# Performance work log

Hardware: AMD Instinct MI355X
Metric: run time of the kernel (lower is better)

## Reference

```python
import jax, jax.numpy as jnp
import numpy as np

NEG_SLOPE = 0.2  # PyG GATConv default leaky_relu slope
N_NODES, N_EDGES, F_IN, HID = 25000, 200000, 64, 128


def gat_layer(x, src, dst, W, a_src, a_dst, b, heads, ch):
    """PyG-style GATConv (concat=True, eval mode). x:[N,Fin] -> [N,heads*ch]."""
    N = x.shape[0]
    h = (x @ W).reshape(N, heads, ch)                      # [N,H,C]
    al_s = jnp.sum(h * a_src, axis=-1)                     # [N,H]
    al_d = jnp.sum(h * a_dst, axis=-1)                     # [N,H]
    e = jax.nn.leaky_relu(al_s[src] + al_d[dst], NEG_SLOPE)  # [E,H]
    # segment softmax over incoming edges of each dst node (stable)
    e = e - jax.ops.segment_max(e, dst, num_segments=N)[dst]
    ex = jnp.exp(e)
    alpha = ex / jax.ops.segment_sum(ex, dst, num_segments=N)[dst]  # [E,H]
    out = jax.ops.segment_sum(h[src] * alpha[:, :, None], dst, num_segments=N)  # [N,H,C]
    return out.reshape(N, heads * ch) + b


def setup_inputs() -> dict:
    key = jax.random.key(0)
    ks = jax.random.split(key, 24)
    def g(k, shape, fan_in):
        return jax.random.normal(k, shape, dtype=jnp.float32) / np.sqrt(fan_in)
    inp = {
        "x": jax.random.normal(ks[0], (N_NODES, F_IN), dtype=jnp.float32),
        "edge_index": jax.random.randint(ks[1], (2, N_EDGES), 0, N_NODES, dtype=jnp.int64) if jax.config.jax_enable_x64 else jax.random.randint(ks[1], (2, N_EDGES), 0, N_NODES).astype(jnp.int32),
        "liquor_idx": jax.random.randint(ks[2], (4096,), 0, N_NODES),
        "ingredient_idx": jax.random.randint(ks[3], (4096,), 0, N_NODES),
        "W1": g(ks[4], (F_IN, 8 * HID), F_IN), "a_s1": g(ks[5], (8, HID), HID), "a_d1": g(ks[6], (8, HID), HID), "b1": jnp.zeros((8 * HID,), jnp.float32),
        "W2": g(ks[7], (8 * HID, 8 * HID), 8 * HID), "a_s2": g(ks[8], (8, HID), HID), "a_d2": g(ks[9], (8, HID), HID), "b2": jnp.zeros((8 * HID,), jnp.float32),
        "W3": g(ks[10], (8 * HID, HID), 8 * HID), "a_s3": g(ks[11], (1, HID), HID), "a_d3": g(ks[12], (1, HID), HID), "b3": jnp.zeros((HID,), jnp.float32),
        # MLP scorer: 256 -> 128 -> 64 -> 1
        "mw1": g(ks[13], (2 * HID, HID), 2 * HID), "mb1": jnp.zeros((HID,), jnp.float32),
        "mw2": g(ks[14], (HID, HID // 2), HID), "mb2": jnp.zeros((HID // 2,), jnp.float32),
        "mw3": g(ks[15], (HID // 2, 1), HID // 2), "mb3": jnp.zeros((1,), jnp.float32),
    }
    return inp


def reference(x, edge_index, liquor_idx, ingredient_idx,
              W1, a_s1, a_d1, b1, W2, a_s2, a_d2, b2, W3, a_s3, a_d3, b3,
              mw1, mb1, mw2, mb2, mw3, mb3):
    N = x.shape[0]
    loops = jnp.arange(N, dtype=edge_index.dtype)  # GATConv adds self-loops
    src = jnp.concatenate([edge_index[0], loops])
    dst = jnp.concatenate([edge_index[1], loops])
    h = jax.nn.relu(gat_layer(x, src, dst, W1, a_s1, a_d1, b1, 8, HID))
    h = jax.nn.relu(gat_layer(h, src, dst, W2, a_s2, a_d2, b2, 8, HID))
    h = gat_layer(h, src, dst, W3, a_s3, a_d3, b3, 1, HID)
    pair = jnp.concatenate([h[liquor_idx], h[ingredient_idx]], axis=-1)  # [B,256]
    z = jax.nn.relu(pair @ mw1 + mb1)
    z = jax.nn.relu(z @ mw2 + mb2)
    z = z @ mw3 + mb3
    return jax.nn.sigmoid(z).squeeze(-1)
```

## Files before the change

kernel.cpp:

```cpp
#include <hip/hip_runtime.h>
#include <math.h>

#define NEG_SLOPE 0.2f

typedef short short8 __attribute__((ext_vector_type(8)));
typedef float f32x4 __attribute__((ext_vector_type(4)));

__device__ __forceinline__ float lrelu(float x){ return x > 0.f ? x : NEG_SLOPE * x; }

__device__ __forceinline__ unsigned short f2bf(float f){
  union { float f; unsigned u; } v; v.f = f;
  unsigned r = v.u + 0x7fff + ((v.u >> 16) & 1);
  return (unsigned short)(r >> 16);
}
__device__ __forceinline__ float bf2f(unsigned short u){
  union { unsigned u; float f; } v; v.u = ((unsigned)u) << 16; return v.f;
}

__device__ __forceinline__ void gld16(const unsigned short* g, unsigned short* l){
  __builtin_amdgcn_global_load_lds(
      (const __attribute__((address_space(1))) unsigned int*)g,
      (__attribute__((address_space(3))) unsigned int*)l, 16, 0, 0);
}

#define MFMA_BF16 __builtin_amdgcn_mfma_f32_16x16x32_bf16

__global__ void k_count(const int* __restrict__ dst, int* __restrict__ cnt, int E){
  int e = blockIdx.x*blockDim.x + threadIdx.x;
  if (e < E) atomicAdd(&cnt[dst[e]], 1);
}

__global__ void k_blockscan(const int* __restrict__ cnt, int* __restrict__ row,
                            int* __restrict__ aux, int n){
  __shared__ int buf[256];
  int t = threadIdx.x;
  int base = blockIdx.x * 256;
  int v = (base + t < n) ? cnt[base + t] : 0;
  buf[t] = v;
  __syncthreads();
  #pragma unroll
  for (int off = 1; off < 256; off <<= 1){
    int u = (t >= off) ? buf[t - off] : 0;
    __syncthreads();
    buf[t] += u;
    __syncthreads();
  }
  if (base + t < n) row[base + t + 1] = buf[t];
  if (t == 255) aux[blockIdx.x] = buf[255];
  if (blockIdx.x == 0 && t == 0) row[0] = 0;
}

__global__ void k_addoff(const int* __restrict__ aux, int* __restrict__ row, int n){
  __shared__ int s_pre;
  int b = blockIdx.x, t = threadIdx.x;
  if (t == 0){
    int pre = 0;
    for (int i = 0; i < b; ++i) pre += aux[i];
    s_pre = pre;
  }
  __syncthreads();
  int i = b * 256 + t;
  if (i < n) row[i + 1] += s_pre;
}

__global__ void k_scatter(const int* __restrict__ src, const int* __restrict__ dst,
                          const int* __restrict__ row, int* __restrict__ cur,
                          int* __restrict__ csr, int E){
  int e = blockIdx.x*blockDim.x + threadIdx.x;
  if (e < E){
    int d = dst[e];
    int p = atomicAdd(&cur[d], 1);
    csr[row[d] + p] = src[e];
  }
}

__global__ void k_prep(const float* __restrict__ x, unsigned short* __restrict__ xb, int nx, int nxb,
                       const float* __restrict__ W1, unsigned short* __restrict__ Wt1,
                       const float* __restrict__ W2, unsigned short* __restrict__ Wt2,
                       const float* __restrict__ W3, unsigned short* __restrict__ Wt3){
  __shared__ float tile[32][33];
  int b = blockIdx.x, t = threadIdx.x;
  if (b < nxb){
    int i0 = b * 2048 + t * 8;
    if (i0 + 8 <= nx){
      float4 f0 = *reinterpret_cast<const float4*>(x + i0);
      float4 f1 = *reinterpret_cast<const float4*>(x + i0 + 4);
      short8 o;
      o[0]=f2bf(f0.x); o[1]=f2bf(f0.y); o[2]=f2bf(f0.z); o[3]=f2bf(f0.w);
      o[4]=f2bf(f1.x); o[5]=f2bf(f1.y); o[6]=f2bf(f1.z); o[7]=f2bf(f1.w);
      *reinterpret_cast<short8*>(xb + i0) = o;
    } else {
      for (int k = 0; k < 8 && i0 + k < nx; ++k) xb[i0 + k] = f2bf(x[i0 + k]);
    }
    return;
  }
  const float* W; unsigned short* Wt; int K, N, ti;
  if (b < nxb + 64)            { W = W1; Wt = Wt1; K = 64;   N = 1024; ti = b - nxb;
                                 int kb = (ti & 1) * 32, nb = (ti >> 1) * 32;
                                 int tx = t & 31, ty = t >> 5;
                                 #pragma unroll
                                 for (int i = ty; i < 32; i += 8) tile[i][tx] = W[(size_t)(kb+i)*N + nb+tx];
                                 __syncthreads();
                                 #pragma unroll
                                 for (int i = ty; i < 32; i += 8) Wt[(size_t)(nb+i)*K + kb+tx] = f2bf(tile[tx][i]);
                                 return; }
  if (b < nxb + 64 + 1024)     { W = W2; Wt = Wt2; K = 1024; N = 1024; ti = b - nxb - 64; }
  else                         { W = W3; Wt = Wt3; K = 1024; N = 128;  ti = b - nxb - 64 - 1024; }
  int kb = (ti & 31) * 32, nb = (ti >> 5) * 32;
  int tx = t & 31, ty = t >> 5;
  #pragma unroll
  for (int i = ty; i < 32; i += 8) tile[i][tx] = W[(size_t)(kb+i)*N + nb+tx];
  __syncthreads();
  #pragma unroll
  for (int i = ty; i < 32; i += 8) Wt[(size_t)(nb+i)*K + kb+tx] = f2bf(tile[tx][i]);
}

__global__ void k_fold(const float* __restrict__ W1, const float* __restrict__ a_s,
                       const float* __restrict__ a_d, float* __restrict__ ws){
  int k = blockIdx.x, t = threadIdx.x;
  int h = t >> 5, l = t & 31;
  float4 wv = *reinterpret_cast<const float4*>(&W1[(size_t)k * 1024 + h * 128 + l * 4]);
  float4 sv = *reinterpret_cast<const float4*>(&a_s[h * 128 + l * 4]);
  float4 dv = *reinterpret_cast<const float4*>(&a_d[h * 128 + l * 4]);
  float ps = wv.x*sv.x + wv.y*sv.y + wv.z*sv.z + wv.w*sv.w;
  float pd = wv.x*dv.x + wv.y*dv.y + wv.z*dv.z + wv.w*dv.w;
  #pragma unroll
  for (int off = 16; off >= 1; off >>= 1){
    ps += __shfl_xor(ps, off);
    pd += __shfl_xor(pd, off);
  }
  if (l == 0){ ws[k * 16 + h] = ps; ws[k * 16 + 8 + h] = pd; }
}

__global__ void k_logits1(const unsigned short* __restrict__ xb, const float* __restrict__ ws,
                          float* __restrict__ ALS, float* __restrict__ ALD, int N){
  __shared__ unsigned short lx[32 * 64];
  __shared__ float lw[64 * 16];
  int t = threadIdx.x;
  int n0 = blockIdx.x * 32;
  int r = t >> 3, c = (t & 7) * 8;
  if (n0 + r < N)
    *reinterpret_cast<short8*>(&lx[r * 64 + c]) =
      *reinterpret_cast<const short8*>(&xb[(size_t)(n0 + r) * 64 + c]);
  else {
    short8 z = {0,0,0,0,0,0,0,0};
    *reinterpret_cast<short8*>(&lx[r * 64 + c]) = z;
  }
  *reinterpret_cast<float4*>(&lw[t * 4]) = *reinterpret_cast<const float4*>(&ws[t * 4]);
  __syncthreads();
  int nl = t >> 3, h = t & 7;
  if (n0 + nl >= N) return;
  float s = 0.f, d = 0.f;
  #pragma unroll 8
  for (int k = 0; k < 64; ++k){
    float xv = bf2f(lx[nl * 64 + k]);
    s = fmaf(xv, lw[k * 16 + h], s);
    d = fmaf(xv, lw[k * 16 + 8 + h], d);
  }
  ALS[(size_t)(n0 + nl) * 8 + h] = s;
  ALD[(size_t)(n0 + nl) * 8 + h] = d;
}

__global__ void k_gat_x(const unsigned short* __restrict__ xb, const float* __restrict__ ALS,
                        const float* __restrict__ ALD, const int* __restrict__ row,
                        const int* __restrict__ csr, unsigned short* __restrict__ G, int N){
  int t = threadIdx.x;
  int n = blockIdx.x * 4 + (t >> 6);
  if (n >= N) return;
  int lane = t & 63;
  float ald[8], m[8], l[8], acc[8];
  float xv = bf2f(xb[(size_t)n * 64 + lane]);
  #pragma unroll
  for (int h = 0; h < 8; ++h){
    ald[h] = ALD[(size_t)n * 8 + h];
    m[h] = lrelu(ALS[(size_t)n * 8 + h] + ald[h]);
    l[h] = 1.f;
    acc[h] = xv;
  }
  int beg = row[n], end = row[n + 1];
  for (int j = beg; j < end; ++j){
    int s = csr[j];
    float xs = bf2f(xb[(size_t)s * 64 + lane]);
    #pragma unroll
    for (int h = 0; h < 8; ++h){
      float e = lrelu(ALS[(size_t)s * 8 + h] + ald[h]);
      float mn = fmaxf(m[h], e);
      float sc = __expf(m[h] - mn);
      float p  = __expf(e - mn);
      acc[h] = acc[h] * sc + p * xs;
      l[h]   = l[h] * sc + p;
      m[h]   = mn;
    }
  }
  #pragma unroll
  for (int h = 0; h < 8; ++h)
    G[(size_t)n * 512 + h * 64 + lane] = f2bf(acc[h] / l[h]);
}

__global__ __launch_bounds__(256) void k_gemm_g(
    const unsigned short* __restrict__ G,
    const unsigned short* __restrict__ Bt,
    const float* __restrict__ bias,
    unsigned short* __restrict__ C,
    int M){
  __shared__ unsigned short As[128 * 32];
  __shared__ unsigned short Bs[128 * 32];
  const int nwg = gridDim.x;
  int bid = blockIdx.x;
  int swz = ((nwg & 7) == 0) ? ((bid & 7) * (nwg >> 3) + (bid >> 3)) : bid;
  const int head = swz % 8, byi = swz / 8;
  const int bm = byi * 128, bn = head * 128;
  const int tid  = threadIdx.x;
  const int lane = tid & 63, wave = tid >> 6;
  const int wr = wave >> 1, wc = wave & 1;
  const int lr = lane & 15, lk = lane >> 4;
  const int srow = wave * 16 + (lane >> 2);
  const int skc  = (lane & 3) * 8;
  int ar0 = bm + srow;      if (ar0 >= M) ar0 = M - 1;
  int ar1 = bm + srow + 64; if (ar1 >= M) ar1 = M - 1;
  const unsigned short* ga0 = G + (size_t)ar0 * 512 + head * 64 + skc;
  const unsigned short* ga1 = G + (size_t)ar1 * 512 + head * 64 + skc;
  const unsigned short* gb0 = Bt + (size_t)(bn + srow) * 64 + skc;
  const unsigned short* gb1 = Bt + (size_t)(bn + srow + 64) * 64 + skc;
  f32x4 acc[4][4] = {};
  #pragma unroll
  for (int k0 = 0; k0 < 64; k0 += 32){
    gld16(ga0 + k0, &As[(size_t)wave * 512]);
    gld16(ga1 + k0, &As[(size_t)(wave + 4) * 512]);
    gld16(gb0 + k0, &Bs[(size_t)wave * 512]);
    gld16(gb1 + k0, &Bs[(size_t)(wave + 4) * 512]);
    __syncthreads();
    short8 af[4], bg[4];
    #pragma unroll
    for (int m = 0; m < 4; ++m)
      af[m] = *reinterpret_cast<const short8*>(&As[(wr * 64 + m * 16 + lr) * 32 + lk * 8]);
    #pragma unroll
    for (int n = 0; n < 4; ++n)
      bg[n] = *reinterpret_cast<const short8*>(&Bs[(wc * 64 + n * 16 + lr) * 32 + lk * 8]);
    #pragma unroll
    for (int m = 0; m < 4; ++m)
      #pragma unroll
      for (int n = 0; n < 4; ++n)
        acc[m][n] = MFMA_BF16(af[m], bg[n], acc[m][n], 0, 0, 0);
    __syncthreads();
  }
  float bv[4];
  #pragma unroll
  for (int n = 0; n < 4; ++n) bv[n] = bias[bn + wc * 64 + n * 16 + lr];
  #pragma unroll
  for (int m = 0; m < 4; ++m){
    #pragma unroll
    for (int j = 0; j < 4; ++j){
      int rowi = bm + wr * 64 + m * 16 + lk * 4 + j;
      if (rowi < M){
        #pragma unroll
        for (int n = 0; n < 4; ++n)
          C[(size_t)rowi * 1024 + bn + wc * 64 + n * 16 + lr] = f2bf(fmaxf(acc[m][n][j] + bv[n], 0.f));
      }
    }
  }
}

template<int HEADS>
__global__ __launch_bounds__(256) void k_gemm_fused(
    const unsigned short* __restrict__ A, const unsigned short* __restrict__ Bt,
    unsigned short* __restrict__ C,
    const float* __restrict__ a_s, const float* __restrict__ a_d,
    float* __restrict__ ALS, float* __restrict__ ALD,
    int M, int N, int K, int gxc){
  __shared__ unsigned short SMEM[2 * 128 * 32];
  unsigned short* As = SMEM;
  unsigned short* Bs = SMEM + 128 * 32;
  const int nwg = gridDim.x;
  int bid = blockIdx.x;
  int swz = ((nwg & 7) == 0) ? ((bid & 7) * (nwg >> 3) + (bid >> 3)) : bid;
  const int bxi = swz % gxc, byi = swz / gxc;
  const int bm = byi * 128, bn = bxi * 128;
  const int head = bxi;
  const int tid  = threadIdx.x;
  const int lane = tid & 63, wave = tid >> 6;
  const int wr = wave >> 1, wc = wave & 1;
  const int lr = lane & 15, lk = lane >> 4;
  const int srow = wave * 16 + (lane >> 2);
  const int skc  = (lane & 3) * 8;
  int ar0 = bm + srow;      if (ar0 >= M) ar0 = M - 1;
  int ar1 = bm + srow + 64; if (ar1 >= M) ar1 = M - 1;
  const unsigned short* ga0 = A  + (size_t)ar0 * K + skc;
  const unsigned short* ga1 = A  + (size_t)ar1 * K + skc;
  const unsigned short* gb0 = Bt + (size_t)(bn + srow) * K + skc;
  const unsigned short* gb1 = Bt + (size_t)(bn + srow + 64) * K + skc;
  f32x4 acc[4][4] = {};
  for (int k0 = 0; k0 < K; k0 += 32){
    gld16(ga0 + k0, &As[(size_t)wave * 512]);
    gld16(ga1 + k0, &As[(size_t)(wave + 4) * 512]);
    gld16(gb0 + k0, &Bs[(size_t)wave * 512]);
    gld16(gb1 + k0, &Bs[(size_t)(wave + 4) * 512]);
    __syncthreads();
    short8 af[4], bg[4];
    #pragma unroll
    for (int m = 0; m < 4; ++m)
      af[m] = *reinterpret_cast<const short8*>(&As[(wr * 64 + m * 16 + lr) * 32 + lk * 8]);
    #pragma unroll
    for (int n = 0; n < 4; ++n)
      bg[n] = *reinterpret_cast<const short8*>(&Bs[(wc * 64 + n * 16 + lr) * 32 + lk * 8]);
    #pragma unroll
    for (int m = 0; m < 4; ++m)
      #pragma unroll
      for (int n = 0; n < 4; ++n)
        acc[m][n] = MFMA_BF16(af[m], bg[n], acc[m][n], 0, 0, 0);
    __syncthreads();
  }
  #pragma unroll
  for (int m = 0; m < 4; ++m){
    #pragma unroll
    for (int j = 0; j < 4; ++j){
      int rowi = bm + wr * 64 + m * 16 + lk * 4 + j;
      if (rowi < M){
        #pragma unroll
        for (int n = 0; n < 4; ++n)
          C[(size_t)rowi * N + bn + wc * 64 + n * 16 + lr] = f2bf(acc[m][n][j]);
      }
    }
  }
  float as4[4], ad4[4];
  #pragma unroll
  for (int n = 0; n < 4; ++n){
    as4[n] = a_s[head * 128 + wc * 64 + n * 16 + lr];
    ad4[n] = a_d[head * 128 + wc * 64 + n * 16 + lr];
  }
  float* red = (float*)SMEM;
  #pragma unroll
  for (int m = 0; m < 4; ++m){
    #pragma unroll
    for (int j = 0; j < 4; ++j){
      float ps = 0.f;
      #pragma unroll
      for (int n = 0; n < 4; ++n) ps = fmaf(acc[m][n][j], as4[n], ps);
      red[(wr * 64 + m * 16 + lk * 4 + j) * 32 + wc * 16 + lr] = ps;
    }
  }
  __syncthreads();
  if (tid < 128){
    float s = 0.f;
    #pragma unroll
    for (int i = 0; i < 32; ++i) s += red[tid * 32 + ((i + tid) & 31)];
    int gr = bm + tid;
    if (gr < M) ALS[(size_t)gr * HEADS + head] = s;
  }
  __syncthreads();
  #pragma unroll
  for (int m = 0; m < 4; ++m){
    #pragma unroll
    for (int j = 0; j < 4; ++j){
      float pd = 0.f;
      #pragma unroll
      for (int n = 0; n < 4; ++n) pd = fmaf(acc[m][n][j], ad4[n], pd);
      red[(wr * 64 + m * 16 + lk * 4 + j) * 32 + wc * 16 + lr] = pd;
    }
  }
  __syncthreads();
  if (tid < 128){
    float s = 0.f;
    #pragma unroll
    for (int i = 0; i < 32; ++i) s += red[tid * 32 + ((i + tid) & 31)];
    int gr = bm + tid;
    if (gr < M) ALD[(size_t)gr * HEADS + head] = s;
  }
}

__global__ __launch_bounds__(512, 2) void k_gemm256p8(
    const unsigned short* __restrict__ A,
    const unsigned short* __restrict__ Bt,
    unsigned short* __restrict__ C,
    const float* __restrict__ a_s, const float* __restrict__ a_d,
    float* __restrict__ ALS, float* __restrict__ ALD,
    int M, int N, int K, int gxc){
  __shared__ unsigned short smem[2 * 32768];
  const int nwg = gridDim.x;
  int bid = blockIdx.x;
  int swz = ((nwg & 7) == 0) ? ((bid & 7) * (nwg >> 3) + (bid >> 3)) : bid;
  const int bxi = swz % gxc, byi = swz / gxc;
  const int bm = byi * 256, bn = bxi * 256;
  const int tid = threadIdx.x;
  const int lane = tid & 63, wave = tid >> 6;
  const int wr = wave >> 2, wc = wave & 3;
  const int lr = lane & 15, lk = lane >> 4;
  const int sr = tid >> 3;
  const int scol = ((tid & 7) << 3) ^ ((sr & 7) << 3);
  unsigned offA[4], offB[4];
  #pragma unroll
  for (int u = 0; u < 4; ++u){
    int r = bm + u * 64 + sr; if (r >= M) r = M - 1;
    offA[u] = (unsigned)r * (unsigned)K + scol;
    offB[u] = (unsigned)(bn + u * 64 + sr) * (unsigned)K + scol;
  }
  const int wdst = wave * 512;
  const int NKT = K >> 6;
  const int NIT = NKT >> 1;

  #define STA(T,u) gld16(A  + (size_t)offA[u] + (size_t)(T)*64, &smem[((T)&1)*32768 + (u)*4096 + wdst])
  #define STB(T,u) gld16(Bt + (size_t)offB[u] + (size_t)(T)*64, &smem[((T)&1)*32768 + 16384 + (u)*4096 + wdst])

  #pragma unroll
  for (int u = 0; u < 4; ++u) STA(0, u);
  #pragma unroll
  for (int u = 0; u < 4; ++u) STB(0, u);
  #pragma unroll
  for (int u = 0; u < 4; ++u) STA(1, u);
  asm volatile("s_waitcnt vmcnt(4)" ::: "memory");
  __builtin_amdgcn_s_barrier();

  f32x4 acc[8][4] = {};
  short8 af[4][2], bg[4][2];

  #define RD_A(moff) \
    _Pragma("unroll") \
    for (int m = 0; m < 4; ++m){ \
      int row = wr * 128 + (m + (moff)) * 16 + lr; \
      int rb = row * 64, sw = (row & 7) << 3; \
      af[m][0] = *reinterpret_cast<const short8*>(&sa[rb + ((lk * 8) ^ sw)]); \
      af[m][1] = *reinterpret_cast<const short8*>(&sa[rb + ((32 + lk * 8) ^ sw)]); \
    }
  #define RD_B(n0_, n1_) \
    _Pragma("unroll") \
    for (int n = (n0_); n < (n1_); ++n){ \
      int row = wc * 64 + n * 16 + lr; \
      int rb = row * 64, sw = (row & 7) << 3; \
      bg[n][0] = *reinterpret_cast<const short8*>(&sb[rb + ((lk * 8) ^ sw)]); \
      bg[n][1] = *reinterpret_cast<const short8*>(&sb[rb + ((32 + lk * 8) ^ sw)]); \
    }
  #define SYNC_MFMA_BEG \
    __builtin_amdgcn_s_barrier(); \
    asm volatile("s_waitcnt lgkmcnt(0)" ::: "memory"); \
    __builtin_amdgcn_sched_barrier(0); \
    __builtin_amdgcn_s_setprio(1);
  #define QUAD(mb, nb) \
    _Pragma("unroll") \
    for (int m = 0; m < 4; ++m) \
      _Pragma("unroll") \
      for (int n = 0; n < 2; ++n){ \
        acc[(mb)+m][(nb)+n] = MFMA_BF16(af[m][0], bg[(nb)+n][0], acc[(mb)+m][(nb)+n], 0, 0, 0); \
        acc[(mb)+m][(nb)+n] = MFMA_BF16(af[m][1], bg[(nb)+n][1], acc[(mb)+m][(nb)+n], 0, 0, 0); \
      }
  #define SYNC_MFMA_END \
    __builtin_amdgcn_s_setprio(0); \
    __builtin_amdgcn_s_barrier();

  for (int it = 0; it < NIT; ++it){
    const int T = it << 1;
    {
      const unsigned short* sa = &smem[(T & 1) * 32768];
      const unsigned short* sb = sa + 16384;
      RD_A(0); RD_B(0, 2);
      STB(T + 1, 0); STB(T + 1, 1);
      SYNC_MFMA_BEG; QUAD(0, 0); SYNC_MFMA_END;
      RD_B(2, 4);
      STB(T + 1, 2); STB(T + 1, 3);
      SYNC_MFMA_BEG; QUAD(0, 2); SYNC_MFMA_END;
      RD_A(4);
      if (T + 2 < NKT){ STA(T + 2, 0); STA(T + 2, 2); }
      SYNC_MFMA_BEG; QUAD(4, 0); SYNC_MFMA_END;
      if (T + 2 < NKT){ STA(T + 2, 1); STA(T + 2, 3); }
      __builtin_amdgcn_s_barrier();
      __builtin_amdgcn_s_setprio(1);
      QUAD(4, 2);
      __builtin_amdgcn_s_setprio(0);
      asm volatile("s_waitcnt vmcnt(4)" ::: "memory");
      __builtin_amdgcn_s_barrier();
    }
    {
      const unsigned short* sa = &smem[((T + 1) & 1) * 32768];
      const unsigned short* sb = sa + 16384;
      RD_A(0); RD_B(0, 2);
      if (T + 2 < NKT){ STB(T + 2, 0); STB(T + 2, 1); }
      SYNC_MFMA_BEG; QUAD(0, 0); SYNC_MFMA_END;
      RD_B(2, 4);
      if (T + 2 < NKT){ STB(T + 2, 2); STB(T + 2, 3); }
      SYNC_MFMA_BEG; QUAD(0, 2); SYNC_MFMA_END;
      RD_A(4);
      if (T + 3 < NKT){ STA(T + 3, 0); STA(T + 3, 2); }
      SYNC_MFMA_BEG; QUAD(4, 0); SYNC_MFMA_END;
      if (T + 3 < NKT){ STA(T + 3, 1); STA(T + 3, 3); }
      __builtin_amdgcn_s_barrier();
      __builtin_amdgcn_s_setprio(1);
      QUAD(4, 2);
      __builtin_amdgcn_s_setprio(0);
      asm volatile("s_waitcnt vmcnt(4)" ::: "memory");
      __builtin_amdgcn_s_barrier();
    }
  }

  #pragma unroll
  for (int m = 0; m < 8; ++m){
    #pragma unroll
    for (int j = 0; j < 4; ++j){
      int row = bm + wr * 128 + m * 16 + lk * 4 + j;
      if (row < M){
        #pragma unroll
        for (int n = 0; n < 4; ++n)
          C[(size_t)row * N + bn + wc * 64 + n * 16 + lr] = f2bf(acc[m][n][j]);
      }
    }
  }
  const int hloc = wc >> 1;
  float as4[4], ad4[4];
  #pragma unroll
  for (int n = 0; n < 4; ++n){
    as4[n] = a_s[(bxi * 2 + hloc) * 128 + (wc & 1) * 64 + n * 16 + lr];
    ad4[n] = a_d[(bxi * 2 + hloc) * 128 + (wc & 1) * 64 + n * 16 + lr];
  }
  float2* red = (float2*)smem;
  __syncthreads();
  #pragma unroll
  for (int hh = 0; hh < 2; ++hh){
    if (hloc == hh){
      #pragma unroll
      for (int m = 0; m < 8; ++m){
        #pragma unroll
        for (int j = 0; j < 4; ++j){
          float ps = 0.f, pd = 0.f;
          #pragma unroll
          for (int n = 0; n < 4; ++n){
            ps = fmaf(acc[m][n][j], as4[n], ps);
            pd = fmaf(acc[m][n][j], ad4[n], pd);
          }
          red[(wr * 128 + m * 16 + lk * 4 + j) * 32 + (wc & 1) * 16 + lr] = make_float2(ps, pd);
        }
      }
    }
    __syncthreads();
    if (tid < 256){
      float ss = 0.f, sd = 0.f;
      #pragma unroll
      for (int i = 0; i < 32; ++i){
        float2 v = red[tid * 32 + ((i + tid) & 31)];
        ss += v.x; sd += v.y;
      }
      int gr = bm + tid;
      if (gr < M){
        ALS[(size_t)gr * 8 + bxi * 2 + hh] = ss;
        ALD[(size_t)gr * 8 + bxi * 2 + hh] = sd;
      }
    }
    __syncthreads();
  }
  #undef STA
  #undef STB
  #undef RD_A
  #undef RD_B
  #undef SYNC_MFMA_BEG
  #undef QUAD
  #undef SYNC_MFMA_END
}

template<int HEADS, int VEC, int OUTBF>
__global__ void k_gat_bf(const unsigned short* __restrict__ hp, const float* __restrict__ al_s,
                         const float* __restrict__ al_d, const int* __restrict__ row,
                         const int* __restrict__ csr, const float* __restrict__ bias,
                         void* __restrict__ outv, int N, int do_relu){
  constexpr int TPH = 128 / VEC;
  int n = blockIdx.x;
  int t = threadIdx.x;
  int h = t / TPH;
  int c0 = (t % TPH) * VEC;
  float ald = al_d[(size_t)n * HEADS + h];
  float mA = lrelu(al_s[(size_t)n * HEADS + h] + ald);
  float lA = 1.f;
  float accA[VEC], accB[VEC];
  float mB = -1e30f, lB = 0.f;
  const unsigned short* hpn = hp + ((size_t)n * HEADS + h) * 128 + c0;
  if constexpr (VEC == 8){
    short8 hv8 = *reinterpret_cast<const short8*>(hpn);
    #pragma unroll
    for (int v = 0; v < 8; ++v){ accA[v] = bf2f((unsigned short)hv8[v]); accB[v] = 0.f; }
  } else {
    ushort2 hv2 = *reinterpret_cast<const ushort2*>(hpn);
    accA[0] = bf2f(hv2.x); accA[1] = bf2f(hv2.y);
    accB[0] = 0.f; accB[1] = 0.f;
  }
  int beg = row[n], end = row[n + 1];
  int j = beg;
  for (; j + 1 < end; j += 2){
    int s0 = csr[j], s1 = csr[j + 1];
    float e0 = lrelu(al_s[(size_t)s0 * HEADS + h] + ald);
    float e1 = lrelu(al_s[(size_t)s1 * HEADS + h] + ald);
    const unsigned short* p0 = hp + ((size_t)s0 * HEADS + h) * 128 + c0;
    const unsigned short* p1 = hp + ((size_t)s1 * HEADS + h) * 128 + c0;
    if constexpr (VEC == 8){
      short8 v0 = *reinterpret_cast<const short8*>(p0);
      short8 v1 = *reinterpret_cast<const short8*>(p1);
      float mn0 = fmaxf(mA, e0), mn1 = fmaxf(mB, e1);
      float sc0 = __expf(mA - mn0), sc1 = __expf(mB - mn1);
      float pw0 = __expf(e0 - mn0), pw1 = __expf(e1 - mn1);
      #pragma unroll
      for (int v = 0; v < 8; ++v){
        accA[v] = accA[v] * sc0 + pw0 * bf2f((unsigned short)v0[v]);
        accB[v] = accB[v] * sc1 + pw1 * bf2f((unsigned short)v1[v]);
      }
      lA = lA * sc0 + pw0; mA = mn0;
      lB = lB * sc1 + pw1; mB = mn1;
    } else {
      ushort2 v0 = *reinterpret_cast<const ushort2*>(p0);
      ushort2 v1 = *reinterpret_cast<const ushort2*>(p1);
      float mn0 = fmaxf(mA, e0), mn1 = fmaxf(mB, e1);
      float sc0 = __expf(mA - mn0), sc1 = __expf(mB - mn1);
      float pw0 = __expf(e0 - mn0), pw1 = __expf(e1 - mn1);
      accA[0] = accA[0] * sc0 + pw0 * bf2f(v0.x);
      accA[1] = accA[1] * sc0 + pw0 * bf2f(v0.y);
      accB[0] = accB[0] * sc1 + pw1 * bf2f(v1.x);
      accB[1] = accB[1] * sc1 + pw1 * bf2f(v1.y);
      lA = lA * sc0 + pw0; mA = mn0;
      lB = lB * sc1 + pw1; mB = mn1;
    }
  }
  if (j < end){
    int s0 = csr[j];
    float e0 = lrelu(al_s[(size_t)s0 * HEADS + h] + ald);
    const unsigned short* p0 = hp + ((size_t)s0 * HEADS + h) * 128 + c0;
    float mn0 = fmaxf(mA, e0);
    float sc0 = __expf(mA - mn0), pw0 = __expf(e0 - mn0);
    if constexpr (VEC == 8){
      short8 v0 = *reinterpret_cast<const short8*>(p0);
      #pragma unroll
      for (int v = 0; v < 8; ++v) accA[v] = accA[v] * sc0 + pw0 * bf2f((unsigned short)v0[v]);
    } else {
      ushort2 v0 = *reinterpret_cast<const ushort2*>(p0);
      accA[0] = accA[0] * sc0 + pw0 * bf2f(v0.x);
      accA[1] = accA[1] * sc0 + pw0 * bf2f(v0.y);
    }
    lA = lA * sc0 + pw0; mA = mn0;
  }
  float mn = fmaxf(mA, mB);
  float sA = __expf(mA - mn), sB = __expf(mB - mn);
  float l = lA * sA + lB * sB;
  float inv = 1.f / l;
  size_t ob = ((size_t)n * HEADS + h) * 128 + c0;
  #pragma unroll
  for (int v = 0; v < VEC; ++v){
    float o = (accA[v] * sA + accB[v] * sB) * inv + bias[h * 128 + c0 + v];
    if (do_relu) o = fmaxf(o, 0.f);
    if constexpr (OUTBF) ((unsigned short*)outv)[ob + v] = f2bf(o);
    else                 ((float*)outv)[ob + v] = o;
  }
}

__global__ void k_gat3(const unsigned short* __restrict__ hp, const float* __restrict__ al_s,
                       const float* __restrict__ al_d, const int* __restrict__ row,
                       const int* __restrict__ csr, const float* __restrict__ bias,
                       const int* __restrict__ liq, const int* __restrict__ ing,
                       float* __restrict__ out, int NB){
  int b = blockIdx.x;
  int n = (b < NB) ? liq[b] : ing[b - NB];
  int t = threadIdx.x;
  int c0 = t * 2;
  float ald = al_d[n];
  float m = lrelu(al_s[n] + ald);
  float l = 1.f;
  ushort2 hv2 = *reinterpret_cast<const ushort2*>(hp + (size_t)n * 128 + c0);
  float a0 = bf2f(hv2.x), a1 = bf2f(hv2.y);
  int beg = row[n], end = row[n + 1];
  for (int j = beg; j < end; ++j){
    int s = csr[j];
    float e = lrelu(al_s[s] + ald);
    float mn = fmaxf(m, e);
    float sc = __expf(m - mn), p = __expf(e - mn);
    ushort2 v = *reinterpret_cast<const ushort2*>(hp + (size_t)s * 128 + c0);
    a0 = a0 * sc + p * bf2f(v.x);
    a1 = a1 * sc + p * bf2f(v.y);
    l = l * sc + p;
    m = mn;
  }
  float inv = 1.f / l;
  out[(size_t)b * 128 + c0]     = a0 * inv + bias[c0];
  out[(size_t)b * 128 + c0 + 1] = a1 * inv + bias[c0 + 1];
}

__global__ void k_mlp(const float* __restrict__ h3,
                      const float* __restrict__ mw1, const float* __restrict__ mb1,
                      const float* __restrict__ mw2, const float* __restrict__ mb2,
                      const float* __restrict__ mw3, const float* __restrict__ mb3,
                      float* __restrict__ out, int B){
  __shared__ float pairv[256];
  __shared__ float z1[128];
  __shared__ float z2[64];
  int r = blockIdx.x;
  int t = threadIdx.x;
  pairv[t]       = h3[(size_t)r * 128 + t];
  pairv[128 + t] = h3[(size_t)(B + r) * 128 + t];
  __syncthreads();
  float a1 = mb1[t];
  for (int k = 0; k < 256; ++k) a1 = fmaf(pairv[k], mw1[k * 128 + t], a1);
  z1[t] = fmaxf(a1, 0.f);
  __syncthreads();
  if (t < 64){
    float a2 = mb2[t];
    for (int k = 0; k < 128; ++k) a2 = fmaf(z1[k], mw2[k * 64 + t], a2);
    z2[t] = fmaxf(a2, 0.f);
  }
  __syncthreads();
  if (t < 64){
    float p = z2[t] * mw3[t];
    #pragma unroll
    for (int off = 32; off >= 1; off >>= 1) p += __shfl_xor(p, off);
    if (t == 0) out[r] = 1.f / (1.f + __expf(-(p + mb3[0])));
  }
}

extern "C" void kernel_launch(void* const* d_in, const int* in_sizes, int n_in,
                              void* d_out, int out_size, void* d_ws, size_t ws_size,
                              hipStream_t stream){
  const float* x   = (const float*)d_in[0];
  const int*   ei  = (const int*)  d_in[1];
  const int*   liq = (const int*)  d_in[2];
  const int*   ing = (const int*)  d_in[3];
  const float* W1  = (const float*)d_in[4];
  const float* as1 = (const float*)d_in[5];
  const float* ad1 = (const float*)d_in[6];
  const float* b1  = (const float*)d_in[7];
  const float* W2  = (const float*)d_in[8];
  const float* as2 = (const float*)d_in[9];
  const float* ad2 = (const float*)d_in[10];
  const float* b2  = (const float*)d_in[11];
  const float* W3  = (const float*)d_in[12];
  const float* as3 = (const float*)d_in[13];
  const float* ad3 = (const float*)d_in[14];
  const float* b3  = (const float*)d_in[15];
  const float* mw1 = (const float*)d_in[16];
  const float* mb1 = (const float*)d_in[17];
  const float* mw2 = (const float*)d_in[18];
  const float* mb2 = (const float*)d_in[19];
  const float* mw3 = (const float*)d_in[20];
  const float* mb3 = (const float*)d_in[21];
  float* out = (float*)d_out;

  const int N = in_sizes[0] / 64;
  const int E = in_sizes[1] / 2;
  const int B = in_sizes[2];
  const int* srcp = ei;
  const int* dstp = ei + E;

  char* w = (char*)d_ws;
  auto alloc = [&](size_t bytes) -> char* {
    char* p = w;
    w += (bytes + 255) & ~(size_t)255;
    return p;
  };
  unsigned short* P    = (unsigned short*)alloc((size_t)N * 1024 * 2);
  unsigned short* Hb   = (unsigned short*)alloc((size_t)N * 1024 * 2);
  float*          H3   = (float*)         alloc((size_t)2 * B * 128 * 4);
  unsigned short* xb   = (unsigned short*)alloc((size_t)N * 64 * 2);
  unsigned short* Wt1  = (unsigned short*)alloc((size_t)1024 * 64 * 2);
  unsigned short* Wt2  = (unsigned short*)alloc((size_t)1024 * 1024 * 2);
  unsigned short* Wt3  = (unsigned short*)alloc((size_t)128 * 1024 * 2);
  float* ALS  = (float*)alloc((size_t)N * 8 * 4);
  float* ALD  = (float*)alloc((size_t)N * 8 * 4);
  float* ws1  = (float*)alloc((size_t)64 * 16 * 4);
  int*   row  = (int*)  alloc((size_t)(N + 1) * 4);
  int*   cntcur = (int*)alloc((size_t)2 * N * 4);
  int*   cnt  = cntcur;
  int*   cur  = cntcur + N;
  int*   aux  = (int*)  alloc((size_t)256 * 4);
  int*   csr  = (int*)  alloc((size_t)E * 4);
  unsigned short* G = P;
  (void)ws_size; (void)n_in; (void)out_size;

  int nx = N * 64;
  int nxb = (nx + 2047) / 2048;
  k_prep<<<nxb + 64 + 1024 + 128, 256, 0, stream>>>(x, xb, nx, nxb, W1, Wt1, W2, Wt2, W3, Wt3);
  k_fold<<<64, 256, 0, stream>>>(W1, as1, ad1, ws1);

  hipMemsetAsync(cntcur, 0, (size_t)2 * N * 4, stream);
  int eb = (E + 255) / 256;
  int nb = (N + 255) / 256;
  k_count<<<eb, 256, 0, stream>>>(dstp, cnt, E);
  k_blockscan<<<nb, 256, 0, stream>>>(cnt, row, aux, N);
  k_addoff<<<nb, 256, 0, stream>>>(aux, row, N);
  k_scatter<<<eb, 256, 0, stream>>>(srcp, dstp, row, cur, csr, E);

  const int mt  = (N + 127) / 128;
  const int mt2 = (N + 255) / 256;

  k_logits1<<<(N + 31) / 32, 256, 0, stream>>>(xb, ws1, ALS, ALD, N);
  k_gat_x<<<(N + 3) / 4, 256, 0, stream>>>(xb, ALS, ALD, row, csr, G, N);
  k_gemm_g<<<8 * mt, 256, 0, stream>>>(G, Wt1, b1, Hb, N);

  k_gemm256p8<<<4 * mt2, 512, 0, stream>>>(Hb, Wt2, P, as2, ad2, ALS, ALD, N, 1024, 1024, 4);
  k_gat_bf<8,8,1><<<N, 128, 0, stream>>>(P, ALS, ALD, row, csr, b2, Hb, N, 1);

  k_gemm_fused<1><<<1 * mt, 256, 0, stream>>>(Hb, Wt3, P, as3, ad3, ALS, ALD, N, 128, 1024, 1);
  k_gat3<<<2 * B, 64, 0, stream>>>(P, ALS, ALD, row, csr, b3, liq, ing, H3, B);

  k_mlp<<<B, 128, 0, stream>>>(H3, mw1, mb1, mw2, mb2, mw3, mb3, out, B);
}
```

Baseline: 333.2 us.

## Precompute edge softmax weights in separate pass instead of online softmax in aggregation

Adds a k_sm kernel per layer that computes per-edge exponentiated attention weights, the self-loop weight and the inverse normaliser using a two-pass max/sum over each node's incoming edges. The aggregation kernels then become plain weighted FMA sums with no exp or rescale per edge and no per-head redundant exp across channel lanes. It also parallelises the prefix-offset sum in k_addoff with a tree reduction. The cost is three extra launches and writing and reading an E×8 float alpha buffer. Layer 3 now computes softmax for all N nodes even though only 2B nodes are aggregated.

```diff
diff --git a/kernel.cpp b/kernel.cpp
--- a/kernel.cpp
+++ b/kernel.cpp
@@ -51,16 +51,17 @@
 }
 
 __global__ void k_addoff(const int* __restrict__ aux, int* __restrict__ row, int n){
-  __shared__ int s_pre;
+  __shared__ int sbuf[256];
   int b = blockIdx.x, t = threadIdx.x;
-  if (t == 0){
-    int pre = 0;
-    for (int i = 0; i < b; ++i) pre += aux[i];
-    s_pre = pre;
-  }
-  __syncthreads();
+  sbuf[t] = (t < b) ? aux[t] : 0;
+  __syncthreads();
+  #pragma unroll
+  for (int off = 128; off >= 1; off >>= 1){
+    if (t < off) sbuf[t] += sbuf[t + off];
+    __syncthreads();
+  }
   int i = b * 256 + t;
-  if (i < n) row[i + 1] += s_pre;
+  if (i < n) row[i + 1] += sbuf[0];
 }
 
 __global__ void k_scatter(const int* __restrict__ src, const int* __restrict__ dst,
@@ -161,40 +162,64 @@
   ALD[(size_t)(n0 + nl) * 8 + h] = d;
 }
 
-__global__ void k_gat_x(const unsigned short* __restrict__ xb, const float* __restrict__ ALS,
-                        const float* __restrict__ ALD, const int* __restrict__ row,
-                        const int* __restrict__ csr, unsigned short* __restrict__ G, int N){
+template<int HEADS>
+__global__ void k_sm(const float* __restrict__ ALS, const float* __restrict__ ALD,
+                     const int* __restrict__ row, const int* __restrict__ csr,
+                     float* __restrict__ alpha, float* __restrict__ alps,
+                     float* __restrict__ invl, int N){
+  int idx = blockIdx.x * blockDim.x + threadIdx.x;
+  int n = idx / HEADS, h = idx - n * HEADS;
+  if (n >= N) return;
+  float ald = ALD[(size_t)n * HEADS + h];
+  float es = lrelu(ALS[(size_t)n * HEADS + h] + ald);
+  float m = es;
+  int beg = row[n], end = row[n + 1];
+  for (int j = beg; j < end; ++j)
+    m = fmaxf(m, lrelu(ALS[(size_t)csr[j] * HEADS + h] + ald));
+  float ps = __expf(es - m);
+  float l = ps;
+  for (int j = beg; j < end; ++j){
+    float p = __expf(lrelu(ALS[(size_t)csr[j] * HEADS + h] + ald) - m);
+    alpha[(size_t)j * HEADS + h] = p;
+    l += p;
+  }
+  alps[(size_t)n * HEADS + h] = ps;
+  invl[(size_t)n * HEADS + h] = 1.f / l;
+}
+
+__global__ void k_gat_x(const unsigned short* __restrict__ xb, const float* __restrict__ alpha,
+                        const float* __restrict__ alps, const float* __restrict__ invl,
+                        const int* __restrict__ row, const int* __restrict__ csr,
+                        unsigned short* __restrict__ G, int N){
   int t = threadIdx.x;
   int n = blockIdx.x * 4 + (t >> 6);
   if (n >= N) return;
   int lane = t & 63;
-  float ald[8], m[8], l[8], acc[8];
   float xv = bf2f(xb[(size_t)n * 64 + lane]);
-  #pragma unroll
-  for (int h = 0; h < 8; ++h){
-    ald[h] = ALD[(size_t)n * 8 + h];
-    m[h] = lrelu(ALS[(size_t)n * 8 + h] + ald[h]);
-    l[h] = 1.f;
-    acc[h] = xv;
-  }
+  float4 s0 = *reinterpret_cast<const float4*>(&alps[(size_t)n * 8]);
+  float4 s1 = *reinterpret_cast<const float4*>(&alps[(size_t)n * 8 + 4]);
+  float acc[8] = {s0.x*xv, s0.y*xv, s0.z*xv, s0.w*xv, s1.x*xv, s1.y*xv, s1.z*xv, s1.w*xv};
   int beg = row[n], end = row[n + 1];
   for (int j = beg; j < end; ++j){
     int s = csr[j];
     float xs = bf2f(xb[(size_t)s * 64 + lane]);
-    #pragma unroll
-    for (int h = 0; h < 8; ++h){
-      float e = lrelu(ALS[(size_t)s * 8 + h] + ald[h]);
-      float mn = fmaxf(m[h], e);
-      float sc = __expf(m[h] - mn);
-      float p  = __expf(e - mn);
-      acc[h] = acc[h] * sc + p * xs;
-      l[h]   = l[h] * sc + p;
-      m[h]   = mn;
-    }
-  }
+    float4 a0 = *reinterpret_cast<const float4*>(&alpha[(size_t)j * 8]);
+    float4 a1 = *reinterpret_cast<const float4*>(&alpha[(size_t)j * 8 + 4]);
+    acc[0] = fmaf(a0.x, xs, acc[0]);
+    acc[1] = fmaf(a0.y, xs, acc[1]);
+    acc[2] = fmaf(a0.z, xs, acc[2]);
+    acc[3] = fmaf(a0.w, xs, acc[3]);
+    acc[4] = fmaf(a1.x, xs, acc[4]);
+    acc[5] = fmaf(a1.y, xs, acc[5]);
+    acc[6] = fmaf(a1.z, xs, acc[6]);
+    acc[7] = fmaf(a1.w, xs, acc[7]);
+  }
+  float4 i0 = *reinterpret_cast<const float4*>(&invl[(size_t)n * 8]);
+  float4 i1 = *reinterpret_cast<const float4*>(&invl[(size_t)n * 8 + 4]);
+  float iv[8] = {i0.x, i0.y, i0.z, i0.w, i1.x, i1.y, i1.z, i1.w};
   #pragma unroll
   for (int h = 0; h < 8; ++h)
-    G[(size_t)n * 512 + h * 64 + lane] = f2bf(acc[h] / l[h]);
+    G[(size_t)n * 512 + h * 64 + lane] = f2bf(acc[h] * iv[h]);
 }
 
 __global__ __launch_bounds__(256) void k_gemm_g(
@@ -553,124 +578,72 @@
   #undef SYNC_MFMA_END
 }
 
-template<int HEADS, int VEC, int OUTBF>
-__global__ void k_gat_bf(const unsigned short* __restrict__ hp, const float* __restrict__ al_s,
-                         const float* __restrict__ al_d, const int* __restrict__ row,
-                         const int* __restrict__ csr, const float* __restrict__ bias,
-                         void* __restrict__ outv, int N, int do_relu){
-  constexpr int TPH = 128 / VEC;
+__global__ void k_gat2(const unsigned short* __restrict__ hp, const float* __restrict__ alpha,
+                       const float* __restrict__ alps, const float* __restrict__ invl,
+                       const int* __restrict__ row, const int* __restrict__ csr,
+                       const float* __restrict__ bias, unsigned short* __restrict__ outv, int N){
   int n = blockIdx.x;
   int t = threadIdx.x;
-  int h = t / TPH;
-  int c0 = (t % TPH) * VEC;
-  float ald = al_d[(size_t)n * HEADS + h];
-  float mA = lrelu(al_s[(size_t)n * HEADS + h] + ald);
-  float lA = 1.f;
-  float accA[VEC], accB[VEC];
-  float mB = -1e30f, lB = 0.f;
-  const unsigned short* hpn = hp + ((size_t)n * HEADS + h) * 128 + c0;
-  if constexpr (VEC == 8){
-    short8 hv8 = *reinterpret_cast<const short8*>(hpn);
-    #pragma unroll
-    for (int v = 0; v < 8; ++v){ accA[v] = bf2f((unsigned short)hv8[v]); accB[v] = 0.f; }
-  } else {
-    ushort2 hv2 = *reinterpret_cast<const ushort2*>(hpn);
-    accA[0] = bf2f(hv2.x); accA[1] = bf2f(hv2.y);
-    accB[0] = 0.f; accB[1] = 0.f;
-  }
+  int h = t >> 4;
+  int c0 = (t & 15) * 8;
+  float sp = alps[(size_t)n * 8 + h];
+  const unsigned short* hpn = hp + ((size_t)n * 8 + h) * 128 + c0;
+  short8 hv8 = *reinterpret_cast<const short8*>(hpn);
+  float accA[8], accB[8] = {};
+  #pragma unroll
+  for (int v = 0; v < 8; ++v) accA[v] = sp * bf2f((unsigned short)hv8[v]);
   int beg = row[n], end = row[n + 1];
   int j = beg;
   for (; j + 1 < end; j += 2){
     int s0 = csr[j], s1 = csr[j + 1];
-    float e0 = lrelu(al_s[(size_t)s0 * HEADS + h] + ald);
-    float e1 = lrelu(al_s[(size_t)s1 * HEADS + h] + ald);
-    const unsigned short* p0 = hp + ((size_t)s0 * HEADS + h) * 128 + c0;
-    const unsigned short* p1 = hp + ((size_t)s1 * HEADS + h) * 128 + c0;
-    if constexpr (VEC == 8){
-      short8 v0 = *reinterpret_cast<const short8*>(p0);
-      short8 v1 = *reinterpret_cast<const short8*>(p1);
-      float mn0 = fmaxf(mA, e0), mn1 = fmaxf(mB, e1);
-      float sc0 = __expf(mA - mn0), sc1 = __expf(mB - mn1);
-      float pw0 = __expf(e0 - mn0), pw1 = __expf(e1 - mn1);
-      #pragma unroll
-      for (int v = 0; v < 8; ++v){
-        accA[v] = accA[v] * sc0 + pw0 * bf2f((unsigned short)v0[v]);
-        accB[v] = accB[v] * sc1 + pw1 * bf2f((unsigned short)v1[v]);
-      }
-      lA = lA * sc0 + pw0; mA = mn0;
-      lB = lB * sc1 + pw1; mB = mn1;
-    } else {
-      ushort2 v0 = *reinterpret_cast<const ushort2*>(p0);
-      ushort2 v1 = *reinterpret_cast<const ushort2*>(p1);
-      float mn0 = fmaxf(mA, e0), mn1 = fmaxf(mB, e1);
-      float sc0 = __expf(mA - mn0), sc1 = __expf(mB - mn1);
-      float pw0 = __expf(e0 - mn0), pw1 = __expf(e1 - mn1);
-      accA[0] = accA[0] * sc0 + pw0 * bf2f(v0.x);
-      accA[1] = accA[1] * sc0 + pw0 * bf2f(v0.y);
-      accB[0] = accB[0] * sc1 + pw1 * bf2f(v1.x);
-      accB[1] = accB[1] * sc1 + pw1 * bf2f(v1.y);
-      lA = lA * sc0 + pw0; mA = mn0;
-      lB = lB * sc1 + pw1; mB = mn1;
+    float p0 = alpha[(size_t)j * 8 + h];
+    float p1 = alpha[(size_t)(j + 1) * 8 + h];
+    short8 v0 = *reinterpret_cast<const short8*>(hp + ((size_t)s0 * 8 + h) * 128 + c0);
+    short8 v1 = *reinterpret_cast<const short8*>(hp + ((size_t)s1 * 8 + h) * 128 + c0);
+    #pragma unroll
+    for (int v = 0; v < 8; ++v){
+      accA[v] = fmaf(p0, bf2f((unsigned short)v0[v]), accA[v]);
+      accB[v] = fmaf(p1, bf2f((unsigned short)v1[v]), accB[v]);
     }
   }
   if (j < end){
     int s0 = csr[j];
-    float e0 = lrelu(al_s[(size_t)s0 * HEADS + h] + ald);
-    const unsigned short* p0 = hp + ((size_t)s0 * HEADS + h) * 128 + c0;
-    float mn0 = fmaxf(mA, e0);
-    float sc0 = __expf(mA - mn0), pw0 = __expf(e0 - mn0);
-    if constexpr (VEC == 8){
-      short8 v0 = *reinterpret_cast<const short8*>(p0);
-      #pragma unroll
-      for (int v = 0; v < 8; ++v) accA[v] = accA[v] * sc0 + pw0 * bf2f((unsigned short)v0[v]);
-    } else {
-      ushort2 v0 = *reinterpret_cast<const ushort2*>(p0);
-      accA[0] = accA[0] * sc0 + pw0 * bf2f(v0.x);
-      accA[1] = accA[1] * sc0 + pw0 * bf2f(v0.y);
-    }
-    lA = lA * sc0 + pw0; mA = mn0;
-  }
-  float mn = fmaxf(mA, mB);
-  float sA = __expf(mA - mn), sB = __expf(mB - mn);
-  float l = lA * sA + lB * sB;
-  float inv = 1.f / l;
-  size_t ob = ((size_t)n * HEADS + h) * 128 + c0;
-  #pragma unroll
-  for (int v = 0; v < VEC; ++v){
-    float o = (accA[v] * sA + accB[v] * sB) * inv + bias[h * 128 + c0 + v];
-    if (do_relu) o = fmaxf(o, 0.f);
-    if constexpr (OUTBF) ((unsigned short*)outv)[ob + v] = f2bf(o);
-    else                 ((float*)outv)[ob + v] = o;
-  }
-}
-
-__global__ void k_gat3(const unsigned short* __restrict__ hp, const float* __restrict__ al_s,
-                       const float* __restrict__ al_d, const int* __restrict__ row,
-                       const int* __restrict__ csr, const float* __restrict__ bias,
+    float p0 = alpha[(size_t)j * 8 + h];
+    short8 v0 = *reinterpret_cast<const short8*>(hp + ((size_t)s0 * 8 + h) * 128 + c0);
+    #pragma unroll
+    for (int v = 0; v < 8; ++v) accA[v] = fmaf(p0, bf2f((unsigned short)v0[v]), accA[v]);
+  }
+  float inv = invl[(size_t)n * 8 + h];
+  size_t ob = ((size_t)n * 8 + h) * 128 + c0;
+  #pragma unroll
+  for (int v = 0; v < 8; ++v){
+    float o = fmaxf((accA[v] + accB[v]) * inv + bias[h * 128 + c0 + v], 0.f);
+    outv[ob + v] = f2bf(o);
+  }
+}
+
+__global__ void k_gat3(const unsigned short* __restrict__ hp, const float* __restrict__ alpha,
+                       const float* __restrict__ alps, const float* __restrict__ invl,
+                       const int* __restrict__ row, const int* __restrict__ csr,
+                       const float* __restrict__ bias,
                        const int* __restrict__ liq, const int* __restrict__ ing,
                        float* __restrict__ out, int NB){
   int b = blockIdx.x;
   int n = (b < NB) ? liq[b] : ing[b - NB];
   int t = threadIdx.x;
   int c0 = t * 2;
-  float ald = al_d[n];
-  float m = lrelu(al_s[n] + ald);
-  float l = 1.f;
+  float sp = alps[n];
   ushort2 hv2 = *reinterpret_cast<const ushort2*>(hp + (size_t)n * 128 + c0);
-  float a0 = bf2f(hv2.x), a1 = bf2f(hv2.y);
+  float a0 = sp * bf2f(hv2.x), a1 = sp * bf2f(hv2.y);
   int beg = row[n], end = row[n + 1];
   for (int j = beg; j < end; ++j){
     int s = csr[j];
-    float e = lrelu(al_s[s] + ald);
-    float mn = fmaxf(m, e);
-    float sc = __expf(m - mn), p = __expf(e - mn);
+    float p = alpha[j];
     ushort2 v = *reinterpret_cast<const ushort2*>(hp + (size_t)s * 128 + c0);
-    a0 = a0 * sc + p * bf2f(v.x);
-    a1 = a1 * sc + p * bf2f(v.y);
-    l = l * sc + p;
-    m = mn;
-  }
-  float inv = 1.f / l;
+    a0 = fmaf(p, bf2f(v.x), a0);
+    a1 = fmaf(p, bf2f(v.y), a1);
+  }
+  float inv = invl[n];
   out[(size_t)b * 128 + c0]     = a0 * inv + bias[c0];
   out[(size_t)b * 128 + c0 + 1] = a1 * inv + bias[c0 + 1];
 }
@@ -754,6 +727,9 @@
   unsigned short* Wt3  = (unsigned short*)alloc((size_t)128 * 1024 * 2);
   float* ALS  = (float*)alloc((size_t)N * 8 * 4);
   float* ALD  = (float*)alloc((size_t)N * 8 * 4);
+  float* alpha= (float*)alloc((size_t)E * 8 * 4);
+  float* alps = (float*)alloc((size_t)N * 8 * 4);
+  float* invl = (float*)alloc((size_t)N * 8 * 4);
   float* ws1  = (float*)alloc((size_t)64 * 16 * 4);
   int*   row  = (int*)  alloc((size_t)(N + 1) * 4);
   int*   cntcur = (int*)alloc((size_t)2 * N * 4);
@@ -779,16 +755,21 @@
 
   const int mt  = (N + 127) / 128;
   const int mt2 = (N + 255) / 256;
+  const int smb8 = (N * 8 + 255) / 256;
+  const int smb1 = (N + 255) / 256;
 
   k_logits1<<<(N + 31) / 32, 256, 0, stream>>>(xb, ws1, ALS, ALD, N);
-  k_gat_x<<<(N + 3) / 4, 256, 0, stream>>>(xb, ALS, ALD, row, csr, G, N);
+  k_sm<8><<<smb8, 256, 0, stream>>>(ALS, ALD, row, csr, alpha, alps, invl, N);
+  k_gat_x<<<(N + 3) / 4, 256, 0, stream>>>(xb, alpha, alps, invl, row, csr, G, N);
   k_gemm_g<<<8 * mt, 256, 0, stream>>>(G, Wt1, b1, Hb, N);
 
   k_gemm256p8<<<4 * mt2, 512, 0, stream>>>(Hb, Wt2, P, as2, ad2, ALS, ALD, N, 1024, 1024, 4);
-  k_gat_bf<8,8,1><<<N, 128, 0, stream>>>(P, ALS, ALD, row, csr, b2, Hb, N, 1);
+  k_sm<8><<<smb8, 256, 0, stream>>>(ALS, ALD, row, csr, alpha, alps, invl, N);
+  k_gat2<<<N, 128, 0, stream>>>(P, alpha, alps, invl, row, csr, b2, Hb, N);
 
   k_gemm_fused<1><<<1 * mt, 256, 0, stream>>>(Hb, Wt3, P, as3, ad3, ALS, ALD, N, 128, 1024, 1);
-  k_gat3<<<2 * B, 64, 0, stream>>>(P, ALS, ALD, row, csr, b3, liq, ing, H3, B);
+  k_sm<1><<<smb1, 256, 0, stream>>>(ALS, ALD, row, csr, alpha, alps, invl, N);
+  k_gat3<<<2 * B, 64, 0, stream>>>(P, alpha, alps, invl, row, csr, b3, liq, ing, H3, B);
 
   k_mlp<<<B, 128, 0, stream>>>(H3, mw1, mb1, mw2, mb2, mw3, mb3, out, B);
 }
```

Measured after the change: 332.0 us. Within noise of the previous version (-0.4%).
